# Kernel optimization log

Hardware: AMD Instinct MI355X
Metric: run time of the kernel (lower is better)

The kernel has to match this reference:

```python
import jax, jax.numpy as jnp
import numpy as np

B, S, D = 32, 1024, 1280          # batch, spatial tokens, hidden_size
CROSS = 768                        # cross_attention_dim
HEADS = 20
HD = D // HEADS                    # 64
N_AOE, N_IMG = 16, 16              # disease / anatomy token counts
SCALE = 1.0 / float(np.sqrt(HD))


def _split_heads(x):
    # [B, N, D] -> [B, H, N, HD]
    b, n, _ = x.shape
    return x.reshape(b, n, HEADS, HD).transpose(0, 2, 1, 3)


def _attend(q, k, v):
    # q: [B,H,S,HD], k/v: [B,H,K,HD]  (K is tiny, 16)
    scores = jnp.einsum('bhsd,bhkd->bhsk', q, k) * SCALE
    probs = jax.nn.softmax(scores, axis=-1)
    return jnp.einsum('bhsk,bhkd->bhsd', probs, v)


def setup_inputs() -> dict:
    key = jax.random.key(0)
    ks = jax.random.split(key, 10)
    g = lambda k, shape, sc=0.02: jax.random.normal(k, shape, jnp.float32) * sc
    return {
        'hidden_states': jax.random.normal(ks[0], (B, S, D), jnp.float32),
        'encoder_hidden_states': jax.random.normal(ks[1], (B, N_AOE + N_IMG + 16, CROSS), jnp.float32),
        'w_q': g(ks[2], (D, D)),            # attn.to_q, bias=False
        'w_k': g(ks[3], (D, CROSS)),        # attn.to_k (anatomy branch)
        'w_v': g(ks[4], (D, CROSS)),        # attn.to_v
        'w_k_dis': g(ks[5], (D, CROSS)),    # self.to_k_dis
        'w_v_dis': g(ks[6], (D, CROSS)),    # self.to_v_dis
        'w_gate': g(ks[7], (1, CROSS)),     # gate_modulator (randomized to exercise path; init is zeros)
        'b_gate': jnp.zeros((1,), jnp.float32),
        'anat_gate_logit': jnp.float32(0.0),  # logit(0.5) for block_type='both'
        'dis_gate_logit': jnp.float32(0.0),
        'w_out': g(ks[8], (D, D)),          # attn.to_out[0]
        'b_out': jnp.zeros((D,), jnp.float32),
    }


def reference(hidden_states, encoder_hidden_states, w_q, w_k, w_v, w_k_dis,
              w_v_dis, w_gate, b_gate, anat_gate_logit, dis_gate_logit,
              w_out, b_out):
    residual = hidden_states
    b = hidden_states.shape[0]

    # token splits (delta path disabled: delta_scale == 0.0)
    dis_tokens = encoder_hidden_states[:, :N_AOE, :]
    anat_tokens = encoder_hidden_states[:, N_AOE:N_AOE + N_IMG, :]

    # projections (torch Linear: x @ W^T)
    query = _split_heads(hidden_states @ w_q.T)          # [B,H,S,HD]
    k_anat = _split_heads(anat_tokens @ w_k.T)           # [B,H,16,HD]
    v_anat = _split_heads(anat_tokens @ w_v.T)
    k_dis = _split_heads(dis_tokens @ w_k_dis.T)
    v_dis = _split_heads(dis_tokens @ w_v_dis.T)

    z_anat = _attend(query, k_anat, v_anat)              # [B,H,S,HD]
    z_dis = _attend(query, k_dis, v_dis)

    # severity-driven gate shift
    severity = dis_tokens.mean(axis=1)                   # [B, CROSS]
    shift = (severity @ w_gate.T + b_gate).reshape(b, 1, 1, 1)
    anat_gate = jax.nn.sigmoid(anat_gate_logit - shift)
    dis_gate = jax.nn.sigmoid(dis_gate_logit + shift)

    z_final = anat_gate * z_anat + dis_gate * z_dis      # [B,H,S,HD]

    out = z_final.transpose(0, 2, 1, 3).reshape(b, -1, D)
    out = out @ w_out.T + b_out                          # to_out[0]; to_out[1] is dropout (eval identity)
    out = out + residual                                 # residual_connection=True, rescale_output_factor=1.0
    return out
```

## Files before the change

kernel.cpp:

```cpp
#include <hip/hip_runtime.h>
#include <stdint.h>

#define B_     32
#define S_     1024
#define D_     1280
#define CROSS_ 768
#define NTOK   16
#define SCALE_ 0.125f

typedef __bf16 bf16x8 __attribute__((ext_vector_type(8)));
typedef float  f32x4  __attribute__((ext_vector_type(4)));
typedef unsigned short ushort_t;
typedef unsigned int   uint_t;

__device__ __forceinline__ float b2f(ushort_t h){ return __uint_as_float(((uint_t)h)<<16); }
__device__ __forceinline__ ushort_t f2b(float f){
  uint_t u = __float_as_uint(f);
  u += 0x7FFFu + ((u>>16)&1u);
  return (ushort_t)(u>>16);
}
__device__ __forceinline__ uint_t pk2(float x, float y){
  return (uint_t)f2b(x) | ((uint_t)f2b(y)<<16);
}

__device__ __forceinline__ void gload_lds16(const void* g, void* l){
  __builtin_amdgcn_global_load_lds((const __attribute__((address_space(1))) void*)g,
                                   (__attribute__((address_space(3))) void*)l, 16, 0, 0);
}

__device__ __forceinline__ void decode_tile(int lin, int& m0, int& n0){
  int xcd = lin & 7, slot = lin >> 3;
  int m_tile = xcd + 8*(slot/10);
  int n_tile = slot - (slot/10)*10;
  m0 = m_tile*128; n0 = n_tile*128;
}

struct CvtArgs { const float* src[7]; ushort_t* dst[7]; int n[7]; };
__global__ void cvt_kernel(CvtArgs a){
  int t = blockIdx.y;
  const float* s = a.src[t]; ushort_t* d = a.dst[t]; int n = a.n[t];
  int i = (blockIdx.x*blockDim.x + threadIdx.x)*4;
  if(i >= n) return;
  float4 v = *(const float4*)(s+i);
  uint2 o; o.x = pk2(v.x,v.y); o.y = pk2(v.z,v.w);
  *(uint2*)(d+i) = o;
}

__global__ void cvt_big(const float* __restrict__ s, ushort_t* __restrict__ d, int n){
  int i = (blockIdx.x*blockDim.x + threadIdx.x)*8;
  if(i >= n) return;
  float4 v0 = *(const float4*)(s+i), v1 = *(const float4*)(s+i+4);
  uint4 o = { pk2(v0.x,v0.y), pk2(v0.z,v0.w), pk2(v1.x,v1.y), pk2(v1.z,v1.w) };
  *(uint4*)(d+i) = o;
}

__global__ void gates_kernel(const float* __restrict__ enc,
                             const float* __restrict__ w_gate,
                             const float* __restrict__ b_gate,
                             const float* __restrict__ aLog,
                             const float* __restrict__ dLog,
                             float* __restrict__ gates){
  int b = blockIdx.x, tid = threadIdx.x;
  __shared__ float red[256];
  float acc = 0.f;
  for(int k = tid; k < CROSS_; k += 256){
    float s = 0.f;
    for(int t = 0; t < NTOK; ++t)
      s += enc[(size_t)(b*48 + t)*CROSS_ + k];
    acc += w_gate[k] * s;
  }
  red[tid] = acc; __syncthreads();
  for(int off = 128; off > 0; off >>= 1){
    if(tid < off) red[tid] += red[tid+off];
    __syncthreads();
  }
  if(tid == 0){
    float shift = red[0]*(1.f/16.f) + b_gate[0];
    gates[b*2+0] = 1.f/(1.f+__expf(shift - aLog[0]));
    gates[b*2+1] = 1.f/(1.f+__expf(-(dLog[0] + shift)));
  }
}

__global__ __launch_bounds__(256) void kv_gemm(const ushort_t* __restrict__ enc,
      const ushort_t* __restrict__ wk,  const ushort_t* __restrict__ wv,
      const ushort_t* __restrict__ wkd, const ushort_t* __restrict__ wvd,
      ushort_t* __restrict__ kv){
  __shared__ __align__(16) ushort_t As[128*64];
  __shared__ __align__(16) ushort_t Bs[128*64];
  const int tau = blockIdx.z;
  const ushort_t* W = (tau==0)? wk : (tau==1)? wv : (tau==2)? wkd : wvd;
  const int tok_off = (tau < 2) ? NTOK : 0;
  const int m0 = blockIdx.x*128, n0 = blockIdx.y*128;
  const int tid = threadIdx.x, l = tid & 63, w = tid >> 6;
  const int wm = (w&1)*64, wn = (w>>1)*64;
  const f32x4 fz = {0.f,0.f,0.f,0.f};
  f32x4 acc[4][4];
  #pragma unroll
  for(int i=0;i<4;++i){
    #pragma unroll
    for(int j=0;j<4;++j) acc[i][j] = fz;
  }
  for(int kt = 0; kt < CROSS_/64; ++kt){
    const int k0 = kt*64;
    #pragma unroll
    for(int i=0;i<4;++i){
      int row = (w*4+i)*8 + (l>>3);
      int c   = l & 7;
      int gm  = m0 + row;
      int er  = (gm>>4)*48 + tok_off + (gm&15);
      gload_lds16(enc + (size_t)er*CROSS_ + k0 + c*8, As + (w*4+i)*512);
      gload_lds16(W  + (size_t)(n0+row)*CROSS_ + k0 + c*8, Bs + (w*4+i)*512);
    }
    __syncthreads();
    #pragma unroll
    for(int ks = 0; ks < 64; ks += 32){
      bf16x8 a[4], bq[4];
      #pragma unroll
      for(int i=0;i<4;++i) a[i]  = *(const bf16x8*)&As[(wm+i*16+(l&15))*64 + ks + (l>>4)*8];
      #pragma unroll
      for(int j=0;j<4;++j) bq[j] = *(const bf16x8*)&Bs[(wn+j*16+(l&15))*64 + ks + (l>>4)*8];
      #pragma unroll
      for(int i=0;i<4;++i){
        #pragma unroll
        for(int j=0;j<4;++j)
          acc[i][j] = __builtin_amdgcn_mfma_f32_16x16x32_bf16(a[i], bq[j], acc[i][j], 0,0,0);
      }
    }
    __syncthreads();
  }
  #pragma unroll
  for(int i=0;i<4;++i){
    #pragma unroll
    for(int j=0;j<4;++j){
      #pragma unroll
      for(int r=0;r<4;++r){
        int m = m0 + wm + i*16 + (l>>4)*4 + r;
        int n = n0 + wn + j*16 + (l&15);
        int b = m >> 4, t = m & 15;
        kv[(((size_t)tau*B_ + b)*NTOK + t)*D_ + n] = f2b(acc[i][j][r]);
      }
    }
  }
}

__global__ __launch_bounds__(256,3) void gemm1_attn(
      const ushort_t* __restrict__ X, const ushort_t* __restrict__ Wq,
      const ushort_t* __restrict__ kv, const float* __restrict__ gates,
      ushort_t* __restrict__ Z){
  __shared__ __align__(16) union {
    struct { ushort_t As[128*64]; ushort_t Bs[128*64]; } st;
    struct { union { ushort_t qs[128*132];
                     ushort_t ps[4][64*44]; } u;
             ushort_t ks[2*2*16*72];
             ushort_t vts[2*64*40]; } ep;
  } sm;
  int m0, n0; decode_tile(blockIdx.x, m0, n0);
  const int tid = threadIdx.x, l = tid & 63, w = tid >> 6;
  const int wm = (w&1)*64, wn = (w>>1)*64;
  const int b = m0 >> 10;
  const f32x4 fz = {0.f,0.f,0.f,0.f};
  f32x4 acc[4][4];
  #pragma unroll
  for(int i=0;i<4;++i){
    #pragma unroll
    for(int j=0;j<4;++j) acc[i][j] = fz;
  }
  for(int kt = 0; kt < D_/64; ++kt){
    const int k0 = kt*64;
    #pragma unroll
    for(int i=0;i<4;++i){
      int row = (w*4+i)*8 + (l>>3);
      int c   = l & 7;
      gload_lds16(X  + (size_t)(m0+row)*D_ + k0 + c*8, sm.st.As + (w*4+i)*512);
      gload_lds16(Wq + (size_t)(n0+row)*D_ + k0 + c*8, sm.st.Bs + (w*4+i)*512);
    }
    __syncthreads();
    #pragma unroll
    for(int ks = 0; ks < 64; ks += 32){
      bf16x8 a[4], bq[4];
      #pragma unroll
      for(int i=0;i<4;++i) a[i]  = *(const bf16x8*)&sm.st.As[(wm+i*16+(l&15))*64 + ks + (l>>4)*8];
      #pragma unroll
      for(int j=0;j<4;++j) bq[j] = *(const bf16x8*)&sm.st.Bs[(wn+j*16+(l&15))*64 + ks + (l>>4)*8];
      #pragma unroll
      for(int i=0;i<4;++i){
        #pragma unroll
        for(int j=0;j<4;++j)
          acc[i][j] = __builtin_amdgcn_mfma_f32_16x16x32_bf16(a[i], bq[j], acc[i][j], 0,0,0);
      }
    }
    __syncthreads();
  }
  #pragma unroll
  for(int i=0;i<4;++i){
    #pragma unroll
    for(int j=0;j<4;++j){
      #pragma unroll
      for(int r=0;r<4;++r)
        sm.ep.u.qs[(wm+i*16+(l>>4)*4+r)*132 + wn + j*16 + (l&15)] = f2b(acc[i][j][r]);
    }
  }
  for(int id = tid; id < 512; id += 256){
    int h  = id >> 8, rem = id & 255;
    int tk = rem >> 7, t = (rem>>3)&15, c = rem&7;
    int tensor = tk*2;
    const ushort_t* src = kv + (((size_t)tensor*B_ + b)*NTOK + t)*D_ + n0 + h*64 + c*8;
    *(uint4*)&sm.ep.ks[((h*2+tk)*16 + t)*72 + c*8] = *(const uint4*)src;
  }
  for(int id = tid; id < 512; id += 256){
    int h = id >> 8, rem = id & 255;
    int tp = rem >> 3, c = rem & 7;
    int tensor = (tp < 16) ? 1 : 3;
    int t = tp & 15;
    const ushort_t* src = kv + (((size_t)tensor*B_ + b)*NTOK + t)*D_ + n0 + h*64 + c*8;
    uint4 v = *(const uint4*)src;
    const ushort_t* pv = (const ushort_t*)&v;
    #pragma unroll
    for(int e=0;e<8;++e) sm.ep.vts[(h*64 + c*8 + e)*40 + tp] = pv[e];
  }
  __syncthreads();
  const int h = w >> 1, ws0 = (w&1)*64;
  const float gA = gates[b*2+0], gD = gates[b*2+1];
  f32x4 scA[4], scD[4];
  #pragma unroll
  for(int i=0;i<4;++i){ scA[i] = fz; scD[i] = fz; }
  #pragma unroll
  for(int ks0 = 0; ks0 < 64; ks0 += 32){
    bf16x8 qf[4];
    #pragma unroll
    for(int i=0;i<4;++i)
      qf[i] = *(const bf16x8*)&sm.ep.u.qs[(ws0+i*16+(l&15))*132 + h*64 + ks0 + (l>>4)*8];
    bf16x8 kA = *(const bf16x8*)&sm.ep.ks[((h*2+0)*16 + (l&15))*72 + ks0 + (l>>4)*8];
    bf16x8 kD = *(const bf16x8*)&sm.ep.ks[((h*2+1)*16 + (l&15))*72 + ks0 + (l>>4)*8];
    #pragma unroll
    for(int i=0;i<4;++i){
      scA[i] = __builtin_amdgcn_mfma_f32_16x16x32_bf16(qf[i], kA, scA[i], 0,0,0);
      scD[i] = __builtin_amdgcn_mfma_f32_16x16x32_bf16(qf[i], kD, scD[i], 0,0,0);
    }
  }
  __syncthreads();
  #pragma unroll
  for(int i=0;i<4;++i){
    #pragma unroll
    for(int r=0;r<4;++r){
      float vA = scA[i][r]*SCALE_, vD = scD[i][r]*SCALE_;
      float mA = vA, mD = vD;
      #pragma unroll
      for(int off=1; off<16; off<<=1){
        mA = fmaxf(mA, __shfl_xor(mA, off));
        mD = fmaxf(mD, __shfl_xor(mD, off));
      }
      float eA = __expf(vA - mA), eD = __expf(vD - mD);
      float sA = eA, sD = eD;
      #pragma unroll
      for(int off=1; off<16; off<<=1){
        sA += __shfl_xor(sA, off);
        sD += __shfl_xor(sD, off);
      }
      int lr = i*16 + (l>>4)*4 + r;
      sm.ep.u.ps[w][lr*44 + 0  + (l&15)] = f2b(gA*eA/sA);
      sm.ep.u.ps[w][lr*44 + 16 + (l&15)] = f2b(gD*eD/sD);
    }
  }
  f32x4 z[4][4];
  #pragma unroll
  for(int i=0;i<4;++i){
    #pragma unroll
    for(int j=0;j<4;++j) z[i][j] = fz;
  }
  bf16x8 pa[4], vb[4];
  #pragma unroll
  for(int i=0;i<4;++i) pa[i] = *(const bf16x8*)&sm.ep.u.ps[w][(i*16+(l&15))*44 + (l>>4)*8];
  #pragma unroll
  for(int j=0;j<4;++j) vb[j] = *(const bf16x8*)&sm.ep.vts[(h*64 + j*16 + (l&15))*40 + (l>>4)*8];
  #pragma unroll
  for(int i=0;i<4;++i){
    #pragma unroll
    for(int j=0;j<4;++j)
      z[i][j] = __builtin_amdgcn_mfma_f32_16x16x32_bf16(pa[i], vb[j], z[i][j], 0,0,0);
  }
  #pragma unroll
  for(int i=0;i<4;++i){
    #pragma unroll
    for(int j=0;j<4;++j){
      #pragma unroll
      for(int r=0;r<4;++r){
        int row = m0 + ws0 + i*16 + (l>>4)*4 + r;
        int col = n0 + h*64 + j*16 + (l&15);
        Z[(size_t)row*D_ + col] = f2b(z[i][j][r]);
      }
    }
  }
}

#define VMW(n)  asm volatile("s_waitcnt vmcnt(" #n ")" ::: "memory")
#define FENCE() asm volatile("" ::: "memory")
#define BARX()  do{ FENCE(); __builtin_amdgcn_s_barrier(); FENCE(); }while(0)

__device__ __forceinline__ void stage_aq(const ushort_t* __restrict__ g,
                                         ushort_t* le, int tid){
  int row = tid >> 3;
  int c   = ((tid & 7) ^ (row & 7)) << 3;
  gload_lds16(g + (size_t)row*D_ + c, le + (tid>>6)*512);
}
__device__ __forceinline__ void stage_b2(const ushort_t* __restrict__ g,
                                         ushort_t* lh, int s0, int tid){
  int w   = tid >> 6;
  int blk = w >> 2;
  int t   = tid & 255;
  int rr  = s0 + blk*64 + (t >> 3);
  int c   = ((t & 7) ^ (rr & 7)) << 3;
  gload_lds16(g + (size_t)rr*D_ + c, lh + (s0 + blk*64)*64 + (w&3)*512);
}

__global__ __launch_bounds__(512,2) void gemm2_8p(
      const ushort_t* __restrict__ Zin, const ushort_t* __restrict__ Wo,
      const float* __restrict__ bias, const float* __restrict__ resid,
      float* __restrict__ out){
  __shared__ __align__(16) ushort_t lds[65536];
  const int lid = (blockIdx.x & 7)*80 + (blockIdx.x >> 3);
  const int m0 = (lid/5)*256, n0 = (lid%5)*256;
  const int tid = threadIdx.x, l = tid & 63, w = tid >> 6;
  const int wr = w >> 2, wc = w & 3;
  const int lr = l & 15;
  const int csw0 = ((l>>4)*8)      ^ ((l&7)<<3);
  const int csw1 = (32+(l>>4)*8)   ^ ((l&7)<<3);
  const int bro  = (wc & 1)*64 + lr;
  const ushort_t* Asrc = Zin + (size_t)m0*D_;
  const ushort_t* Bsrc = Wo  + (size_t)n0*D_;
  const f32x4 fz = {0.f,0.f,0.f,0.f};
  f32x4 acc[8][4];
  #pragma unroll
  for(int i=0;i<8;++i){
    #pragma unroll
    for(int j=0;j<4;++j) acc[i][j] = fz;
  }
  bf16x8 a[4][2], bb[2][2];

#define AB(tt) (lds + ((tt)&1)*16384)
#define BB(tt) (lds + 32768 + ((tt)&1)*16384)
#define ST_S0(tt) { stage_aq(Asrc + (size_t)  0*D_ + (tt)*64, AB(tt),          tid); \
                    stage_aq(Asrc + (size_t)128*D_ + (tt)*64, AB(tt) + 8192,   tid); }
#define ST_S1(tt) { stage_b2(Bsrc + (size_t)  0*D_ + (tt)*64, BB(tt),        0, tid); \
                    stage_b2(Bsrc + (size_t)128*D_ + (tt)*64, BB(tt) + 8192, 0, tid); }
#define ST_S2(tt) { stage_b2(Bsrc + (size_t)  0*D_ + (tt)*64, BB(tt),       32, tid); \
                    stage_b2(Bsrc + (size_t)128*D_ + (tt)*64, BB(tt) + 8192,32, tid); }
#define ST_S3(tt) { stage_aq(Asrc + (size_t) 64*D_ + (tt)*64, AB(tt) + 4096,  tid); \
                    stage_aq(Asrc + (size_t)192*D_ + (tt)*64, AB(tt) + 12288, tid); }
#define DS_A(qi, Ab) { _Pragma("unroll") for(int i=0;i<4;++i){ \
      a[i][0] = *(const bf16x8*)&(Ab)[((qi)*64 + i*16 + lr)*64 + csw0]; \
      a[i][1] = *(const bf16x8*)&(Ab)[((qi)*64 + i*16 + lr)*64 + csw1]; } }
#define DS_B(qj, Bb) { _Pragma("unroll") for(int j=0;j<2;++j){ \
      bb[j][0] = *(const bf16x8*)&(Bb)[(bro + ((qj)*2+j)*16)*64 + csw0]; \
      bb[j][1] = *(const bf16x8*)&(Bb)[(bro + ((qj)*2+j)*16)*64 + csw1]; } }
#define MM(qi,qj) { __builtin_amdgcn_s_setprio(1); \
    _Pragma("unroll") for(int i=0;i<4;++i){ _Pragma("unroll") for(int j=0;j<2;++j){ \
      acc[(qi)*4+i][(qj)*2+j] = __builtin_amdgcn_mfma_f32_16x16x32_bf16(a[i][0], bb[j][0], acc[(qi)*4+i][(qj)*2+j],0,0,0); \
      acc[(qi)*4+i][(qj)*2+j] = __builtin_amdgcn_mfma_f32_16x16x32_bf16(a[i][1], bb[j][1], acc[(qi)*4+i][(qj)*2+j],0,0,0); } } \
    __builtin_amdgcn_s_setprio(0); }

  ST_S0(0); ST_S1(0); ST_S2(0); ST_S3(0);
  VMW(4);
  BARX();
  for(int t = 0; t < 19; ++t){
    const ushort_t* Ab = AB(t) + wr*8192;
    const ushort_t* Bb = BB(t) + (wc>>1)*8192;
    DS_A(0,Ab); DS_B(0,Bb); ST_S0(t+1); VMW(4); BARX(); MM(0,0); BARX();
    DS_B(1,Bb);             ST_S1(t+1); VMW(4); BARX(); MM(0,1); BARX();
    DS_A(1,Ab); DS_B(0,Bb); ST_S2(t+1);         BARX(); MM(1,0); BARX();
    DS_B(1,Bb);             ST_S3(t+1); VMW(4); BARX(); MM(1,1); BARX();
  }
  {
    const ushort_t* Ab = AB(19) + wr*8192;
    const ushort_t* Bb = BB(19) + (wc>>1)*8192;
    DS_A(0,Ab); DS_B(0,Bb); VMW(2); BARX(); MM(0,0); BARX();
    DS_B(1,Bb);             VMW(0); BARX(); MM(0,1); BARX();
    DS_A(1,Ab); DS_B(0,Bb);         BARX(); MM(1,0); BARX();
    DS_B(1,Bb);                             MM(1,1);
  }
  float bj[4];
  #pragma unroll
  for(int j=0;j<4;++j) bj[j] = bias[n0 + wc*64 + j*16 + lr];
  #pragma unroll
  for(int i=0;i<8;++i){
    #pragma unroll
    for(int j=0;j<4;++j){
      #pragma unroll
      for(int r=0;r<4;++r){
        int m = m0 + wr*128 + i*16 + (l>>4)*4 + r;
        int n = n0 + wc*64 + j*16 + lr;
        out[(size_t)m*D_ + n] = acc[i][j][r] + bj[j] + resid[(size_t)m*D_ + n];
      }
    }
  }
#undef AB
#undef BB
#undef ST_S0
#undef ST_S1
#undef ST_S2
#undef ST_S3
#undef DS_A
#undef DS_B
#undef MM
}

extern "C" void kernel_launch(void* const* d_in, const int* in_sizes, int n_in,
                              void* d_out, int out_size, void* d_ws, size_t ws_size,
                              hipStream_t stream){
  const float* hidden = (const float*)d_in[0];
  const float* enc    = (const float*)d_in[1];
  const float* w_q    = (const float*)d_in[2];
  const float* w_k    = (const float*)d_in[3];
  const float* w_v    = (const float*)d_in[4];
  const float* w_kd   = (const float*)d_in[5];
  const float* w_vd   = (const float*)d_in[6];
  const float* w_gate = (const float*)d_in[7];
  const float* b_gate = (const float*)d_in[8];
  const float* aLog   = (const float*)d_in[9];
  const float* dLog   = (const float*)d_in[10];
  const float* w_out  = (const float*)d_in[11];
  const float* b_out  = (const float*)d_in[12];
  float* out = (float*)d_out;

  char* ws = (char*)d_ws;
  ushort_t* z_bf   = (ushort_t*)(ws + 0);
  ushort_t* kv_bf  = (ushort_t*)(ws + 83886080);
  ushort_t* wq_bf  = (ushort_t*)(ws + 89128960);
  ushort_t* wk_bf  = (ushort_t*)(ws + 92405760);
  ushort_t* wv_bf  = (ushort_t*)(ws + 94371840);
  ushort_t* wkd_bf = (ushort_t*)(ws + 96337920);
  ushort_t* wvd_bf = (ushort_t*)(ws + 98304000);
  ushort_t* wo_bf  = (ushort_t*)(ws + 100270080);
  ushort_t* enc_bf = (ushort_t*)(ws + 103546880);
  float*    gates  = (float*)   (ws + 105906176);

  ushort_t* hid_bf = (ushort_t*)d_out;

  CvtArgs ca;
  ca.src[0]=w_q;   ca.dst[0]=wq_bf;  ca.n[0]=D_*D_;
  ca.src[1]=w_k;   ca.dst[1]=wk_bf;  ca.n[1]=D_*CROSS_;
  ca.src[2]=w_v;   ca.dst[2]=wv_bf;  ca.n[2]=D_*CROSS_;
  ca.src[3]=w_kd;  ca.dst[3]=wkd_bf; ca.n[3]=D_*CROSS_;
  ca.src[4]=w_vd;  ca.dst[4]=wvd_bf; ca.n[4]=D_*CROSS_;
  ca.src[5]=w_out; ca.dst[5]=wo_bf;  ca.n[5]=D_*D_;
  ca.src[6]=enc;   ca.dst[6]=enc_bf; ca.n[6]=B_*48*CROSS_;
  cvt_kernel<<<dim3(1600,7), 256, 0, stream>>>(ca);
  cvt_big<<<20480, 256, 0, stream>>>(hidden, hid_bf, B_*S_*D_);

  gates_kernel<<<32, 256, 0, stream>>>(enc, w_gate, b_gate, aLog, dLog, gates);
  kv_gemm<<<dim3(4,10,4), 256, 0, stream>>>(enc_bf, wk_bf, wv_bf, wkd_bf, wvd_bf, kv_bf);
  gemm1_attn<<<2560, 256, 0, stream>>>(hid_bf, wq_bf, kv_bf, gates, z_bf);
  gemm2_8p<<<640, 512, 0, stream>>>(z_bf, wo_bf, b_out, hidden, out);
}
```

Baseline: 697.3 us.

## Move Q-projection+attention onto the pipelined 256x256 8-wave GEMM main loop

Replaces the simple 128x128 Q-projection GEMM, which had a single-buffered LDS loop, with the same double-buffered, swizzled 256x256 main loop already used by the output projection. The attention epilogue is rewritten per wave: each wave stages its own Q slices in a private LDS region, loads K fragments directly from global, and does the softmax and PV product locally without block-wide barriers. This aims to cut the Q GEMM's global traffic and barrier stalls. In exchange it uses larger register tiles (8x4 accumulators plus score arrays) at 2 blocks per CU, and the main loop is shared through a macro.

Measured after the change: 666.4 us. -4.4%, faster.

```diff
diff --git a/kernel.cpp b/kernel.cpp
--- a/kernel.cpp
+++ b/kernel.cpp
@@ -26,13 +26,6 @@
 __device__ __forceinline__ void gload_lds16(const void* g, void* l){
   __builtin_amdgcn_global_load_lds((const __attribute__((address_space(1))) void*)g,
                                    (__attribute__((address_space(3))) void*)l, 16, 0, 0);
-}
-
-__device__ __forceinline__ void decode_tile(int lin, int& m0, int& n0){
-  int xcd = lin & 7, slot = lin >> 3;
-  int m_tile = xcd + 8*(slot/10);
-  int n_tile = slot - (slot/10)*10;
-  m0 = m_tile*128; n0 = n_tile*128;
 }
 
 struct CvtArgs { const float* src[7]; ushort_t* dst[7]; int n[7]; };
@@ -143,159 +136,10 @@
   }
 }
 
-__global__ __launch_bounds__(256,3) void gemm1_attn(
-      const ushort_t* __restrict__ X, const ushort_t* __restrict__ Wq,
-      const ushort_t* __restrict__ kv, const float* __restrict__ gates,
-      ushort_t* __restrict__ Z){
-  __shared__ __align__(16) union {
-    struct { ushort_t As[128*64]; ushort_t Bs[128*64]; } st;
-    struct { union { ushort_t qs[128*132];
-                     ushort_t ps[4][64*44]; } u;
-             ushort_t ks[2*2*16*72];
-             ushort_t vts[2*64*40]; } ep;
-  } sm;
-  int m0, n0; decode_tile(blockIdx.x, m0, n0);
-  const int tid = threadIdx.x, l = tid & 63, w = tid >> 6;
-  const int wm = (w&1)*64, wn = (w>>1)*64;
-  const int b = m0 >> 10;
-  const f32x4 fz = {0.f,0.f,0.f,0.f};
-  f32x4 acc[4][4];
-  #pragma unroll
-  for(int i=0;i<4;++i){
-    #pragma unroll
-    for(int j=0;j<4;++j) acc[i][j] = fz;
-  }
-  for(int kt = 0; kt < D_/64; ++kt){
-    const int k0 = kt*64;
-    #pragma unroll
-    for(int i=0;i<4;++i){
-      int row = (w*4+i)*8 + (l>>3);
-      int c   = l & 7;
-      gload_lds16(X  + (size_t)(m0+row)*D_ + k0 + c*8, sm.st.As + (w*4+i)*512);
-      gload_lds16(Wq + (size_t)(n0+row)*D_ + k0 + c*8, sm.st.Bs + (w*4+i)*512);
-    }
-    __syncthreads();
-    #pragma unroll
-    for(int ks = 0; ks < 64; ks += 32){
-      bf16x8 a[4], bq[4];
-      #pragma unroll
-      for(int i=0;i<4;++i) a[i]  = *(const bf16x8*)&sm.st.As[(wm+i*16+(l&15))*64 + ks + (l>>4)*8];
-      #pragma unroll
-      for(int j=0;j<4;++j) bq[j] = *(const bf16x8*)&sm.st.Bs[(wn+j*16+(l&15))*64 + ks + (l>>4)*8];
-      #pragma unroll
-      for(int i=0;i<4;++i){
-        #pragma unroll
-        for(int j=0;j<4;++j)
-          acc[i][j] = __builtin_amdgcn_mfma_f32_16x16x32_bf16(a[i], bq[j], acc[i][j], 0,0,0);
-      }
-    }
-    __syncthreads();
-  }
-  #pragma unroll
-  for(int i=0;i<4;++i){
-    #pragma unroll
-    for(int j=0;j<4;++j){
-      #pragma unroll
-      for(int r=0;r<4;++r)
-        sm.ep.u.qs[(wm+i*16+(l>>4)*4+r)*132 + wn + j*16 + (l&15)] = f2b(acc[i][j][r]);
-    }
-  }
-  for(int id = tid; id < 512; id += 256){
-    int h  = id >> 8, rem = id & 255;
-    int tk = rem >> 7, t = (rem>>3)&15, c = rem&7;
-    int tensor = tk*2;
-    const ushort_t* src = kv + (((size_t)tensor*B_ + b)*NTOK + t)*D_ + n0 + h*64 + c*8;
-    *(uint4*)&sm.ep.ks[((h*2+tk)*16 + t)*72 + c*8] = *(const uint4*)src;
-  }
-  for(int id = tid; id < 512; id += 256){
-    int h = id >> 8, rem = id & 255;
-    int tp = rem >> 3, c = rem & 7;
-    int tensor = (tp < 16) ? 1 : 3;
-    int t = tp & 15;
-    const ushort_t* src = kv + (((size_t)tensor*B_ + b)*NTOK + t)*D_ + n0 + h*64 + c*8;
-    uint4 v = *(const uint4*)src;
-    const ushort_t* pv = (const ushort_t*)&v;
-    #pragma unroll
-    for(int e=0;e<8;++e) sm.ep.vts[(h*64 + c*8 + e)*40 + tp] = pv[e];
-  }
-  __syncthreads();
-  const int h = w >> 1, ws0 = (w&1)*64;
-  const float gA = gates[b*2+0], gD = gates[b*2+1];
-  f32x4 scA[4], scD[4];
-  #pragma unroll
-  for(int i=0;i<4;++i){ scA[i] = fz; scD[i] = fz; }
-  #pragma unroll
-  for(int ks0 = 0; ks0 < 64; ks0 += 32){
-    bf16x8 qf[4];
-    #pragma unroll
-    for(int i=0;i<4;++i)
-      qf[i] = *(const bf16x8*)&sm.ep.u.qs[(ws0+i*16+(l&15))*132 + h*64 + ks0 + (l>>4)*8];
-    bf16x8 kA = *(const bf16x8*)&sm.ep.ks[((h*2+0)*16 + (l&15))*72 + ks0 + (l>>4)*8];
-    bf16x8 kD = *(const bf16x8*)&sm.ep.ks[((h*2+1)*16 + (l&15))*72 + ks0 + (l>>4)*8];
-    #pragma unroll
-    for(int i=0;i<4;++i){
-      scA[i] = __builtin_amdgcn_mfma_f32_16x16x32_bf16(qf[i], kA, scA[i], 0,0,0);
-      scD[i] = __builtin_amdgcn_mfma_f32_16x16x32_bf16(qf[i], kD, scD[i], 0,0,0);
-    }
-  }
-  __syncthreads();
-  #pragma unroll
-  for(int i=0;i<4;++i){
-    #pragma unroll
-    for(int r=0;r<4;++r){
-      float vA = scA[i][r]*SCALE_, vD = scD[i][r]*SCALE_;
-      float mA = vA, mD = vD;
-      #pragma unroll
-      for(int off=1; off<16; off<<=1){
-        mA = fmaxf(mA, __shfl_xor(mA, off));
-        mD = fmaxf(mD, __shfl_xor(mD, off));
-      }
-      float eA = __expf(vA - mA), eD = __expf(vD - mD);
-      float sA = eA, sD = eD;
-      #pragma unroll
-      for(int off=1; off<16; off<<=1){
-        sA += __shfl_xor(sA, off);
-        sD += __shfl_xor(sD, off);
-      }
-      int lr = i*16 + (l>>4)*4 + r;
-      sm.ep.u.ps[w][lr*44 + 0  + (l&15)] = f2b(gA*eA/sA);
-      sm.ep.u.ps[w][lr*44 + 16 + (l&15)] = f2b(gD*eD/sD);
-    }
-  }
-  f32x4 z[4][4];
-  #pragma unroll
-  for(int i=0;i<4;++i){
-    #pragma unroll
-    for(int j=0;j<4;++j) z[i][j] = fz;
-  }
-  bf16x8 pa[4], vb[4];
-  #pragma unroll
-  for(int i=0;i<4;++i) pa[i] = *(const bf16x8*)&sm.ep.u.ps[w][(i*16+(l&15))*44 + (l>>4)*8];
-  #pragma unroll
-  for(int j=0;j<4;++j) vb[j] = *(const bf16x8*)&sm.ep.vts[(h*64 + j*16 + (l&15))*40 + (l>>4)*8];
-  #pragma unroll
-  for(int i=0;i<4;++i){
-    #pragma unroll
-    for(int j=0;j<4;++j)
-      z[i][j] = __builtin_amdgcn_mfma_f32_16x16x32_bf16(pa[i], vb[j], z[i][j], 0,0,0);
-  }
-  #pragma unroll
-  for(int i=0;i<4;++i){
-    #pragma unroll
-    for(int j=0;j<4;++j){
-      #pragma unroll
-      for(int r=0;r<4;++r){
-        int row = m0 + ws0 + i*16 + (l>>4)*4 + r;
-        int col = n0 + h*64 + j*16 + (l&15);
-        Z[(size_t)row*D_ + col] = f2b(z[i][j][r]);
-      }
-    }
-  }
-}
-
 #define VMW(n)  asm volatile("s_waitcnt vmcnt(" #n ")" ::: "memory")
 #define FENCE() asm volatile("" ::: "memory")
 #define BARX()  do{ FENCE(); __builtin_amdgcn_s_barrier(); FENCE(); }while(0)
+#define LGKM0() asm volatile("s_waitcnt lgkmcnt(0)" ::: "memory")
 
 __device__ __forceinline__ void stage_aq(const ushort_t* __restrict__ g,
                                          ushort_t* le, int tid){
@@ -312,30 +156,6 @@
   int c   = ((t & 7) ^ (rr & 7)) << 3;
   gload_lds16(g + (size_t)rr*D_ + c, lh + (s0 + blk*64)*64 + (w&3)*512);
 }
-
-__global__ __launch_bounds__(512,2) void gemm2_8p(
-      const ushort_t* __restrict__ Zin, const ushort_t* __restrict__ Wo,
-      const float* __restrict__ bias, const float* __restrict__ resid,
-      float* __restrict__ out){
-  __shared__ __align__(16) ushort_t lds[65536];
-  const int lid = (blockIdx.x & 7)*80 + (blockIdx.x >> 3);
-  const int m0 = (lid/5)*256, n0 = (lid%5)*256;
-  const int tid = threadIdx.x, l = tid & 63, w = tid >> 6;
-  const int wr = w >> 2, wc = w & 3;
-  const int lr = l & 15;
-  const int csw0 = ((l>>4)*8)      ^ ((l&7)<<3);
-  const int csw1 = (32+(l>>4)*8)   ^ ((l&7)<<3);
-  const int bro  = (wc & 1)*64 + lr;
-  const ushort_t* Asrc = Zin + (size_t)m0*D_;
-  const ushort_t* Bsrc = Wo  + (size_t)n0*D_;
-  const f32x4 fz = {0.f,0.f,0.f,0.f};
-  f32x4 acc[8][4];
-  #pragma unroll
-  for(int i=0;i<8;++i){
-    #pragma unroll
-    for(int j=0;j<4;++j) acc[i][j] = fz;
-  }
-  bf16x8 a[4][2], bb[2][2];
 
 #define AB(tt) (lds + ((tt)&1)*16384)
 #define BB(tt) (lds + 32768 + ((tt)&1)*16384)
@@ -359,25 +179,181 @@
       acc[(qi)*4+i][(qj)*2+j] = __builtin_amdgcn_mfma_f32_16x16x32_bf16(a[i][1], bb[j][1], acc[(qi)*4+i][(qj)*2+j],0,0,0); } } \
     __builtin_amdgcn_s_setprio(0); }
 
-  ST_S0(0); ST_S1(0); ST_S2(0); ST_S3(0);
-  VMW(4);
+#define MAINLOOP_256(NKT) \
+  ST_S0(0); ST_S1(0); ST_S2(0); ST_S3(0); \
+  VMW(4); \
+  BARX(); \
+  for(int t = 0; t < (NKT)-1; ++t){ \
+    const ushort_t* Ab = AB(t) + wr*8192; \
+    const ushort_t* Bb = BB(t) + (wc>>1)*8192; \
+    DS_A(0,Ab); DS_B(0,Bb); ST_S0(t+1); VMW(4); BARX(); MM(0,0); BARX(); \
+    DS_B(1,Bb);             ST_S1(t+1); VMW(4); BARX(); MM(0,1); BARX(); \
+    DS_A(1,Ab); DS_B(0,Bb); ST_S2(t+1);         BARX(); MM(1,0); BARX(); \
+    DS_B(1,Bb);             ST_S3(t+1); VMW(4); BARX(); MM(1,1); BARX(); \
+  } \
+  { \
+    const ushort_t* Ab = AB((NKT)-1) + wr*8192; \
+    const ushort_t* Bb = BB((NKT)-1) + (wc>>1)*8192; \
+    DS_A(0,Ab); DS_B(0,Bb); VMW(2); BARX(); MM(0,0); BARX(); \
+    DS_B(1,Bb);             VMW(0); BARX(); MM(0,1); BARX(); \
+    DS_A(1,Ab); DS_B(0,Bb);         BARX(); MM(1,0); BARX(); \
+    DS_B(1,Bb);                             MM(1,1); \
+  }
+
+__global__ __launch_bounds__(512,2) void gemm1_attn_8p(
+      const ushort_t* __restrict__ X, const ushort_t* __restrict__ Wq,
+      const ushort_t* __restrict__ kv, const float* __restrict__ gates,
+      ushort_t* __restrict__ Z){
+  __shared__ __align__(16) ushort_t lds[65536];
+  const int lid = (blockIdx.x & 7)*80 + (blockIdx.x >> 3);
+  const int m0 = (lid/5)*256, n0 = (lid%5)*256;
+  const int tid = threadIdx.x, l = tid & 63, w = tid >> 6;
+  const int wr = w >> 2, wc = w & 3;
+  const int lr = l & 15;
+  const int csw0 = ((l>>4)*8)    ^ ((l&7)<<3);
+  const int csw1 = (32+(l>>4)*8) ^ ((l&7)<<3);
+  const int bro  = (wc & 1)*64 + lr;
+  const ushort_t* Asrc = X  + (size_t)m0*D_;
+  const ushort_t* Bsrc = Wq + (size_t)n0*D_;
+  const f32x4 fz = {0.f,0.f,0.f,0.f};
+  f32x4 acc[8][4];
+  #pragma unroll
+  for(int i=0;i<8;++i){
+    #pragma unroll
+    for(int j=0;j<4;++j) acc[i][j] = fz;
+  }
+  bf16x8 a[4][2], bb[2][2];
+
+  MAINLOOP_256(20)
+
   BARX();
-  for(int t = 0; t < 19; ++t){
-    const ushort_t* Ab = AB(t) + wr*8192;
-    const ushort_t* Bb = BB(t) + (wc>>1)*8192;
-    DS_A(0,Ab); DS_B(0,Bb); ST_S0(t+1); VMW(4); BARX(); MM(0,0); BARX();
-    DS_B(1,Bb);             ST_S1(t+1); VMW(4); BARX(); MM(0,1); BARX();
-    DS_A(1,Ab); DS_B(0,Bb); ST_S2(t+1);         BARX(); MM(1,0); BARX();
-    DS_B(1,Bb);             ST_S3(t+1); VMW(4); BARX(); MM(1,1); BARX();
-  }
-  {
-    const ushort_t* Ab = AB(19) + wr*8192;
-    const ushort_t* Bb = BB(19) + (wc>>1)*8192;
-    DS_A(0,Ab); DS_B(0,Bb); VMW(2); BARX(); MM(0,0); BARX();
-    DS_B(1,Bb);             VMW(0); BARX(); MM(0,1); BARX();
-    DS_A(1,Ab); DS_B(0,Bb);         BARX(); MM(1,0); BARX();
-    DS_B(1,Bb);                             MM(1,1);
-  }
+  const int b = m0 >> 10;
+  const float gA = gates[b*2+0], gD = gates[b*2+1];
+  ushort_t* R = lds + w*8192;
+  const ushort_t* kbase = kv + ((size_t)b*NTOK + lr)*D_ + n0 + wc*64 + (l>>4)*8;
+  bf16x8 kA0 = *(const bf16x8*)(kbase);
+  bf16x8 kA1 = *(const bf16x8*)(kbase + 32);
+  bf16x8 kD0 = *(const bf16x8*)(kbase + (size_t)2*B_*NTOK*D_);
+  bf16x8 kD1 = *(const bf16x8*)(kbase + (size_t)2*B_*NTOK*D_ + 32);
+  f32x4 scA[8], scD[8];
+  #pragma unroll
+  for(int i=0;i<8;++i){ scA[i] = fz; scD[i] = fz; }
+  #pragma unroll
+  for(int i=0;i<8;++i){
+    ushort_t* qs = R + (i&1)*1024;
+    #pragma unroll
+    for(int j=0;j<4;++j){
+      #pragma unroll
+      for(int r=0;r<4;++r){
+        int row = (l>>4)*4 + r;
+        int col = j*16 + lr;
+        qs[row*64 + ((((col>>3) ^ (row&7))<<3) | (col&7))] = f2b(acc[i][j][r]);
+      }
+    }
+    LGKM0();
+    bf16x8 af0 = *(const bf16x8*)&qs[lr*64 + ((((l>>4))   ^ (lr&7))<<3)];
+    bf16x8 af1 = *(const bf16x8*)&qs[lr*64 + (((4+(l>>4)) ^ (lr&7))<<3)];
+    scA[i] = __builtin_amdgcn_mfma_f32_16x16x32_bf16(af0, kA0, scA[i], 0,0,0);
+    scA[i] = __builtin_amdgcn_mfma_f32_16x16x32_bf16(af1, kA1, scA[i], 0,0,0);
+    scD[i] = __builtin_amdgcn_mfma_f32_16x16x32_bf16(af0, kD0, scD[i], 0,0,0);
+    scD[i] = __builtin_amdgcn_mfma_f32_16x16x32_bf16(af1, kD1, scD[i], 0,0,0);
+  }
+  uint4 vld[4];
+  #pragma unroll
+  for(int it=0; it<4; ++it){
+    int u = it*64 + l;
+    int tp = u >> 3, c = u & 7;
+    int tensor = (tp < 16) ? 1 : 3;
+    int t = tp & 15;
+    vld[it] = *(const uint4*)(kv + (((size_t)tensor*B_ + b)*NTOK + t)*D_
+                                 + n0 + wc*64 + c*8);
+  }
+  LGKM0();
+  #pragma unroll
+  for(int i=0;i<8;++i){
+    #pragma unroll
+    for(int r=0;r<4;++r){
+      float vA = scA[i][r]*SCALE_, vD = scD[i][r]*SCALE_;
+      float mA = vA, mD = vD;
+      #pragma unroll
+      for(int off=1; off<16; off<<=1){
+        mA = fmaxf(mA, __shfl_xor(mA, off));
+        mD = fmaxf(mD, __shfl_xor(mD, off));
+      }
+      float eA = __expf(vA - mA), eD = __expf(vD - mD);
+      float sA = eA, sD = eD;
+      #pragma unroll
+      for(int off=1; off<16; off<<=1){
+        sA += __shfl_xor(sA, off);
+        sD += __shfl_xor(sD, off);
+      }
+      int lrow = i*16 + (l>>4)*4 + r;
+      R[lrow*44 + lr]      = f2b(gA*eA/sA);
+      R[lrow*44 + 16 + lr] = f2b(gD*eD/sD);
+    }
+  }
+  ushort_t* vts = R + 5632;
+  #pragma unroll
+  for(int it=0; it<4; ++it){
+    int u = it*64 + l;
+    int tp = u >> 3, c = u & 7;
+    const ushort_t* pv = (const ushort_t*)&vld[it];
+    #pragma unroll
+    for(int e=0;e<8;++e) vts[(c*8+e)*40 + tp] = pv[e];
+  }
+  LGKM0();
+  bf16x8 pa[8], vb[4];
+  #pragma unroll
+  for(int i=0;i<8;++i) pa[i] = *(const bf16x8*)&R[(i*16+lr)*44 + (l>>4)*8];
+  #pragma unroll
+  for(int j=0;j<4;++j)  vb[j] = *(const bf16x8*)&vts[(j*16+lr)*40 + (l>>4)*8];
+  f32x4 z[8][4];
+  #pragma unroll
+  for(int i=0;i<8;++i){
+    #pragma unroll
+    for(int j=0;j<4;++j)
+      z[i][j] = __builtin_amdgcn_mfma_f32_16x16x32_bf16(pa[i], vb[j], fz, 0,0,0);
+  }
+  #pragma unroll
+  for(int i=0;i<8;++i){
+    #pragma unroll
+    for(int j=0;j<4;++j){
+      #pragma unroll
+      for(int r=0;r<4;++r){
+        int row = m0 + wr*128 + i*16 + (l>>4)*4 + r;
+        int col = n0 + wc*64 + j*16 + lr;
+        Z[(size_t)row*D_ + col] = f2b(z[i][j][r]);
+      }
+    }
+  }
+}
+
+__global__ __launch_bounds__(512,2) void gemm2_8p(
+      const ushort_t* __restrict__ Zin, const ushort_t* __restrict__ Wo,
+      const float* __restrict__ bias, const float* __restrict__ resid,
+      float* __restrict__ out){
+  __shared__ __align__(16) ushort_t lds[65536];
+  const int lid = (blockIdx.x & 7)*80 + (blockIdx.x >> 3);
+  const int m0 = (lid/5)*256, n0 = (lid%5)*256;
+  const int tid = threadIdx.x, l = tid & 63, w = tid >> 6;
+  const int wr = w >> 2, wc = w & 3;
+  const int lr = l & 15;
+  const int csw0 = ((l>>4)*8)    ^ ((l&7)<<3);
+  const int csw1 = (32+(l>>4)*8) ^ ((l&7)<<3);
+  const int bro  = (wc & 1)*64 + lr;
+  const ushort_t* Asrc = Zin + (size_t)m0*D_;
+  const ushort_t* Bsrc = Wo  + (size_t)n0*D_;
+  const f32x4 fz = {0.f,0.f,0.f,0.f};
+  f32x4 acc[8][4];
+  #pragma unroll
+  for(int i=0;i<8;++i){
+    #pragma unroll
+    for(int j=0;j<4;++j) acc[i][j] = fz;
+  }
+  bf16x8 a[4][2], bb[2][2];
+
+  MAINLOOP_256(20)
+
   float bj[4];
   #pragma unroll
   for(int j=0;j<4;++j) bj[j] = bias[n0 + wc*64 + j*16 + lr];
@@ -393,15 +369,6 @@
       }
     }
   }
-#undef AB
-#undef BB
-#undef ST_S0
-#undef ST_S1
-#undef ST_S2
-#undef ST_S3
-#undef DS_A
-#undef DS_B
-#undef MM
 }
 
 extern "C" void kernel_launch(void* const* d_in, const int* in_sizes, int n_in,
@@ -449,6 +416,6 @@
 
   gates_kernel<<<32, 256, 0, stream>>>(enc, w_gate, b_gate, aLog, dLog, gates);
   kv_gemm<<<dim3(4,10,4), 256, 0, stream>>>(enc_bf, wk_bf, wv_bf, wkd_bf, wvd_bf, kv_bf);
-  gemm1_attn<<<2560, 256, 0, stream>>>(hid_bf, wq_bf, kv_bf, gates, z_bf);
+  gemm1_attn_8p<<<640, 512, 0, stream>>>(hid_bf, wq_bf, kv_bf, gates, z_bf);
   gemm2_8p<<<640, 512, 0, stream>>>(z_bf, wo_bf, b_out, hidden, out);
 }
```
